# Performance work log

Hardware: AMD Instinct MI355X
Metric: run time of the kernel (lower is better)

## Reference

```python
import jax, jax.numpy as jnp
import numpy as np

NUM_EMBEDDINGS = 1024
EMBEDDING_DIM = 256
COMMITMENT_COST = 0.25


def setup_inputs() -> dict:
    key = jax.random.key(0)
    k1, k2 = jax.random.split(key)
    inputs = jax.random.normal(k1, (32, EMBEDDING_DIM, 32, 32), dtype=jnp.float32)
    # nn.Embedding weight init: uniform(-1/K, 1/K)
    embeddings = (jax.random.uniform(k2, (NUM_EMBEDDINGS, EMBEDDING_DIM), dtype=jnp.float32) * 2.0 - 1.0) / NUM_EMBEDDINGS
    return {"inputs": inputs, "embeddings": embeddings}


def reference(inputs, embeddings):
    B, D, H, W = inputs.shape
    K = embeddings.shape[0]
    # [B,D,H,W] -> [N,D] with N = B*H*W
    flat = jnp.transpose(inputs, (0, 2, 3, 1)).reshape(-1, D)
    distances = (jnp.sum(flat * flat, axis=1, keepdims=True)
                 + jnp.sum(embeddings * embeddings, axis=1)
                 - 2.0 * jnp.matmul(flat, embeddings.T))
    encoding_indices = jnp.argmin(distances, axis=1)  # [N]
    # gather codebook vectors (same math as one-hot @ embeddings)
    quantized = embeddings[encoding_indices]  # [N,D]
    quantized = quantized.reshape(B, H, W, D).transpose(0, 3, 1, 2)  # [B,D,H,W]
    e_latent_loss = jnp.mean((jax.lax.stop_gradient(quantized) - inputs) ** 2)
    q_latent_loss = jnp.mean((quantized - jax.lax.stop_gradient(inputs)) ** 2)
    loss = q_latent_loss + COMMITMENT_COST * e_latent_loss
    # straight-through estimator
    quantized_st = inputs + jax.lax.stop_gradient(quantized - inputs)
    # perplexity from one-hot average (counts / N)
    counts = jnp.zeros((K,), dtype=flat.dtype).at[encoding_indices].add(1.0)
    avg_probs = counts / flat.shape[0]
    perplexity = jnp.exp(-jnp.sum(avg_probs * jnp.log(avg_probs + 1e-10)))
    return quantized_st, loss, perplexity, encoding_indices.reshape(B, H, W)
```

## Files before the change

kernel.cpp:

```cpp
#include <hip/hip_runtime.h>


#define NROWS 32768
#define CAPA 16384
#define CAPB 8192
#define GAP_TAU 1e-4f

typedef __attribute__((ext_vector_type(8))) short short8;
typedef __attribute__((ext_vector_type(8))) unsigned short ushort8;
typedef __attribute__((ext_vector_type(4))) float f32x4;
typedef __attribute__((ext_vector_type(4))) unsigned int uint4v;

struct Top4 { float v0, v1, v2, v3; int i0, i1, i2; };

__device__ __forceinline__ void top4_init(Top4& t) {
    t.v0 = t.v1 = t.v2 = t.v3 = 3.4e38f;
    t.i0 = t.i1 = t.i2 = 0x7fffffff;
}
__device__ __forceinline__ void top4_insert(Top4& t, float cv, int ci) {
    if (cv < t.v3) {
        if (cv < t.v2) {
            t.v3 = t.v2;
            if (cv < t.v1) {
                t.v2 = t.v1; t.i2 = t.i1;
                if (cv < t.v0) { t.v1 = t.v0; t.i1 = t.i0; t.v0 = cv; t.i0 = ci; }
                else           { t.v1 = cv; t.i1 = ci; }
            } else { t.v2 = cv; t.i2 = ci; }
        } else { t.v3 = cv; }
    }
}
__device__ __forceinline__ void top4_merge(Top4& t, const Top4& o) {
    top4_insert(t, o.v0, o.i0);
    top4_insert(t, o.v1, o.i1);
    top4_insert(t, o.v2, o.i2);
    t.v3 = fminf(t.v3, o.v3);
}

__device__ __forceinline__ unsigned short bf16_rne(float v) {
    unsigned int u = __float_as_uint(v);
    return (unsigned short)((u + 0x7fffu + ((u >> 16) & 1u)) >> 16);
}
__device__ __forceinline__ float bf16_to_f(unsigned short h) {
    return __uint_as_float(((unsigned int)h) << 16);
}

template <int STRIDE>
__device__ __forceinline__ float np_sumsq256(const float* __restrict__ p) {
    float half[2];
#pragma unroll
    for (int h = 0; h < 2; ++h) {
        float r[8];
#pragma unroll
        for (int j = 0; j < 8; ++j) {
            const float v = p[(size_t)(h * 128 + j) * STRIDE];
            r[j] = __fmul_rn(v, v);
        }
        for (int i = 8; i < 128; i += 8) {
#pragma unroll
            for (int j = 0; j < 8; ++j) {
                const float v = p[(size_t)(h * 128 + i + j) * STRIDE];
                r[j] = __fadd_rn(r[j], __fmul_rn(v, v));
            }
        }
        half[h] = __fadd_rn(__fadd_rn(__fadd_rn(r[0], r[1]), __fadd_rn(r[2], r[3])),
                            __fadd_rn(__fadd_rn(r[4], r[5]), __fadd_rn(r[6], r[7])));
    }
    return __fadd_rn(half[0], half[1]);
}

__global__ void prep_kernel(const float* __restrict__ emb, const float* __restrict__ x,
                            float* __restrict__ ee, float* __restrict__ xx,
                            unsigned short* __restrict__ EhW, unsigned short* __restrict__ ElW) {
    if (blockIdx.x < 4) {
        const int k = blockIdx.x * 256 + threadIdx.x;
        ee[k] = np_sumsq256<1>(emb + (size_t)k * 256);
        return;
    }
    if (blockIdx.x >= 260) {
        const int n = (blockIdx.x - 260) * 256 + threadIdx.x;
        const int b = n >> 10, p = n & 1023;
        xx[n] = np_sumsq256<1024>(x + (size_t)b * 262144 + p);
        return;
    }
    const int eid = (blockIdx.x - 4) * 256 + threadIdx.x;
    const int base = eid * 4;
    float4 v = *(const float4*)(emb + base);
    const float vv[4] = {v.x, v.y, v.z, v.w};
    unsigned short h[4], l[4];
#pragma unroll
    for (int i = 0; i < 4; ++i) {
        h[i] = bf16_rne(vv[i]);
        l[i] = bf16_rne(vv[i] - bf16_to_f(h[i]));
    }
    *(ushort4*)(EhW + base) = make_ushort4(h[0], h[1], h[2], h[3]);
    *(ushort4*)(ElW + base) = make_ushort4(l[0], l[1], l[2], l[3]);
}

__global__ __launch_bounds__(256, 4)
void mfma_argmin_kernel(const float* __restrict__ x,
                        const unsigned short* __restrict__ EhW, const unsigned short* __restrict__ ElW,
                        const float* __restrict__ ee, const float* __restrict__ xx,
                        float* __restrict__ pv0, float* __restrict__ pv1,
                        float* __restrict__ pv2, float* __restrict__ pv3,
                        int* __restrict__ pi0, int* __restrict__ pi1, int* __restrict__ pi2) {
    __shared__ unsigned short Eh_s[128 * 32];
    __shared__ unsigned short El_s[128 * 32];
    __shared__ unsigned short Xh_s[128 * 32];
    __shared__ unsigned short Xl_s[128 * 32];
    __shared__ float eeLds[128];
    __shared__ float mV0[128], mV1[128], mV2[128], mV3[128];
    __shared__ int   mI0[128], mI1[128], mI2[128];

    const int t = threadIdx.x;
    const int w = t >> 6, lane = t & 63;
    const int lane15 = lane & 15, quad = lane >> 4;
    const int nblk = blockIdx.x & 255, cblk = blockIdx.x >> 8;
    const int n0 = nblk * 128, c0 = cblk * 128;
    const int b = n0 >> 10, p0 = n0 & 1023;
    const float* xb = x + (size_t)b * 262144 + p0;

    if (t < 128) eeLds[t] = ee[c0 + t];

    f32x4 acc[4][4];
#pragma unroll
    for (int i = 0; i < 4; ++i)
#pragma unroll
        for (int j = 0; j < 4; ++j) acc[i][j] = (f32x4){0.f, 0.f, 0.f, 0.f};

    for (int dc = 0; dc < 8; ++dc) {
        const int d0 = dc * 32;
        __syncthreads();
#pragma unroll
        for (int iter = 0; iter < 2; ++iter) {
            const int id = iter * 256 + t;
            const int p = id & 127, dblk = id >> 7;
            const float* src = xb + (size_t)(d0 + dblk * 8) * 1024 + p;
            float v[8];
#pragma unroll
            for (int j = 0; j < 8; ++j) v[j] = src[(size_t)j * 1024];
            uint4v uh, ul;
#pragma unroll
            for (int jj = 0; jj < 4; ++jj) {
                const unsigned int u0 = __float_as_uint(v[2 * jj]);
                const unsigned int u1 = __float_as_uint(v[2 * jj + 1]);
                uh[jj] = __builtin_amdgcn_perm(u1, u0, 0x07060302u);
                const float r0 = v[2 * jj]     - __uint_as_float(u0 & 0xFFFF0000u);
                const float r1 = v[2 * jj + 1] - __uint_as_float(u1 & 0xFFFF0000u);
                ul[jj] = __builtin_amdgcn_perm(__float_as_uint(r1), __float_as_uint(r0), 0x07060302u);
            }
            *(uint4v*)&Xh_s[p * 32 + dblk * 8] = uh;
            *(uint4v*)&Xl_s[p * 32 + dblk * 8] = ul;
        }
#pragma unroll
        for (int iter = 0; iter < 2; ++iter) {
            const int id = iter * 256 + t;
            const int row = id >> 2, col = id & 3;
            const size_t g = (size_t)(c0 + row) * 256 + d0 + col * 8;
            *(ushort8*)&Eh_s[row * 32 + col * 8] = *(const ushort8*)(EhW + g);
            *(ushort8*)&El_s[row * 32 + col * 8] = *(const ushort8*)(ElW + g);
        }
        __syncthreads();
        short8 ah[4], al[4], bhf[4], blf[4];
#pragma unroll
        for (int i = 0; i < 4; ++i) {
            const int cr = (w >> 1) * 64 + i * 16 + lane15;
            ah[i] = *(const short8*)&Eh_s[cr * 32 + quad * 8];
            al[i] = *(const short8*)&El_s[cr * 32 + quad * 8];
        }
#pragma unroll
        for (int j = 0; j < 4; ++j) {
            const int nr = (w & 1) * 64 + j * 16 + lane15;
            bhf[j] = *(const short8*)&Xh_s[nr * 32 + quad * 8];
            blf[j] = *(const short8*)&Xl_s[nr * 32 + quad * 8];
        }
#pragma unroll
        for (int i = 0; i < 4; ++i)
#pragma unroll
            for (int j = 0; j < 4; ++j) {
                acc[i][j] = __builtin_amdgcn_mfma_f32_16x16x32_bf16(al[i], bhf[j], acc[i][j], 0, 0, 0);
                acc[i][j] = __builtin_amdgcn_mfma_f32_16x16x32_bf16(ah[i], blf[j], acc[i][j], 0, 0, 0);
                acc[i][j] = __builtin_amdgcn_mfma_f32_16x16x32_bf16(ah[i], bhf[j], acc[i][j], 0, 0, 0);
            }
    }
    Top4 tj[4];
#pragma unroll
    for (int j = 0; j < 4; ++j) {
        const float xxv = xx[n0 + (w & 1) * 64 + j * 16 + lane15];
        Top4 tt; top4_init(tt);
#pragma unroll
        for (int i = 0; i < 4; ++i)
#pragma unroll
            for (int r = 0; r < 4; ++r) {
                const int cl = (w >> 1) * 64 + i * 16 + quad * 4 + r;
                const float t1 = __fadd_rn(xxv, eeLds[cl]);
                const float s = __fmaf_rn(-2.0f, acc[i][j][r], t1);
                top4_insert(tt, s, c0 + cl);
            }
#pragma unroll
        for (int off = 16; off <= 32; off <<= 1) {
            Top4 o;
            o.v0 = __shfl_xor(tt.v0, off, 64); o.i0 = __shfl_xor(tt.i0, off, 64);
            o.v1 = __shfl_xor(tt.v1, off, 64); o.i1 = __shfl_xor(tt.i1, off, 64);
            o.v2 = __shfl_xor(tt.v2, off, 64); o.i2 = __shfl_xor(tt.i2, off, 64);
            o.v3 = __shfl_xor(tt.v3, off, 64);
            top4_merge(tt, o);
        }
        tj[j] = tt;
    }
    __syncthreads();
    if (w >= 2 && quad == 0) {
#pragma unroll
        for (int j = 0; j < 4; ++j) {
            const int idx = (w & 1) * 64 + j * 16 + lane15;
            mV0[idx] = tj[j].v0; mV1[idx] = tj[j].v1; mV2[idx] = tj[j].v2; mV3[idx] = tj[j].v3;
            mI0[idx] = tj[j].i0; mI1[idx] = tj[j].i1; mI2[idx] = tj[j].i2;
        }
    }
    __syncthreads();
    if (w < 2 && quad == 0) {
#pragma unroll
        for (int j = 0; j < 4; ++j) {
            const int idx = w * 64 + j * 16 + lane15;
            Top4 tt = tj[j];
            Top4 o;
            o.v0 = mV0[idx]; o.v1 = mV1[idx]; o.v2 = mV2[idx]; o.v3 = mV3[idx];
            o.i0 = mI0[idx]; o.i1 = mI1[idx]; o.i2 = mI2[idx];
            top4_merge(tt, o);
            const size_t g = (size_t)cblk * NROWS + n0 + idx;
            pv0[g] = tt.v0; pv1[g] = tt.v1; pv2[g] = tt.v2; pv3[g] = tt.v3;
            pi0[g] = tt.i0; pi1[g] = tt.i1; pi2[g] = tt.i2;
        }
    }
}

__global__ void combine_kernel(const float* __restrict__ pv0, const float* __restrict__ pv1,
                               const float* __restrict__ pv2, const float* __restrict__ pv3,
                               const int* __restrict__ pi0, const int* __restrict__ pi1,
                               const int* __restrict__ pi2,
                               int* __restrict__ fidx, float* __restrict__ outIdx,
                               int* __restrict__ counts,
                               int* __restrict__ listA, int* __restrict__ nA,
                               int* __restrict__ listB, int* __restrict__ nB) {
    const int n = blockIdx.x * blockDim.x + threadIdx.x;
    if (n >= NROWS) return;
    float v0[8], v1[8], v2[8]; int i0[8], i1[8], i2[8];
    float b1 = 3.4e38f, v4m = 3.4e38f;
#pragma unroll
    for (int s = 0; s < 8; ++s) {
        const size_t g = (size_t)s * NROWS + n;
        v0[s] = pv0[g]; v1[s] = pv1[g]; v2[s] = pv2[g];
        i0[s] = pi0[g]; i1[s] = pi1[g]; i2[s] = pi2[g];
        b1 = fminf(b1, v0[s]);
        v4m = fminf(v4m, pv3[g]);
    }
    if (v4m - b1 < GAP_TAU) {
        const int s = atomicAdd(nB, 1);
        if (s < CAPB) { listB[s] = n; return; }
    } else {
        int ks[24]; int cnt = 0;
#pragma unroll
        for (int s = 0; s < 8; ++s) {
            if (v0[s] - b1 < GAP_TAU) ks[cnt++] = i0[s];
            if (v1[s] - b1 < GAP_TAU) ks[cnt++] = i1[s];
            if (v2[s] - b1 < GAP_TAU) ks[cnt++] = i2[s];
        }
        if (cnt > 1) {
            const int slot = atomicAdd(nA, 1);
            if (slot < CAPA) {
                int* e = listA + (size_t)slot * 32;
                e[0] = n; e[1] = cnt;
                for (int c = 0; c < cnt; ++c) e[2 + c] = ks[c];
                return;
            }
            const int s2 = atomicAdd(nB, 1);
            if (s2 < CAPB) { listB[s2] = n; return; }
        }
        const int bi = ks[0];
        fidx[n] = bi;
        outIdx[n] = (float)bi;
        atomicAdd(&counts[bi], 1);
        return;
    }
    int bi = 0x7fffffff;
#pragma unroll
    for (int s = 0; s < 8; ++s) if (v0[s] == b1 && i0[s] < bi) bi = i0[s];
    fidx[n] = bi; outIdx[n] = (float)bi; atomicAdd(&counts[bi], 1);
}

__global__ __launch_bounds__(256)
void exact_kernel(const float* __restrict__ x, const float* __restrict__ emb,
                  const float* __restrict__ ee, const float* __restrict__ xx,
                  const int* __restrict__ listA, const int* __restrict__ nA,
                  int* __restrict__ fidx, float* __restrict__ outIdx,
                  int* __restrict__ counts) {
    int total = *nA; if (total > CAPA) total = CAPA;
    const int sub = threadIdx.x >> 5;
    const int li  = threadIdx.x & 31;
    for (int e = blockIdx.x * 8 + sub; e < total; e += gridDim.x * 8) {
        const int* ent = listA + (size_t)e * 32;
        const int n = ent[0], cnt = ent[1];
        float s = 3.4e38f; int k = 0x7fffffff;
        if (li < cnt) {
            k = ent[2 + li];
            const int b = n >> 10, p = n & 1023;
            const float* xr = x + (size_t)b * 262144 + p;
            const float* er = emb + (size_t)k * 256;
            float dot = 0.f;
#pragma unroll 8
            for (int d = 0; d < 256; ++d)
                dot = __fmaf_rn(er[d], xr[(size_t)d * 1024], dot);
            s = __fmaf_rn(-2.0f, dot, __fadd_rn(xx[n], ee[k]));
        }
#pragma unroll
        for (int off = 1; off < 32; off <<= 1) {
            const float ov = __shfl_xor(s, off, 32);
            const int   ok = __shfl_xor(k, off, 32);
            if (ov < s || (ov == s && ok < k)) { s = ov; k = ok; }
        }
        if (li == 0) { fidx[n] = k; outIdx[n] = (float)k; atomicAdd(&counts[k], 1); }
    }
}

__global__ __launch_bounds__(256)
void rescanB_kernel(const float* __restrict__ x, const float* __restrict__ emb,
                    const float* __restrict__ ee, const float* __restrict__ xx,
                    const int* __restrict__ listB, const int* __restrict__ nB,
                    int* __restrict__ fidx, float* __restrict__ outIdx,
                    int* __restrict__ counts) {
    __shared__ float xrow[256];
    __shared__ float bV[4];
    __shared__ int   bI[4];
    int total = *nB; if (total > CAPB) total = CAPB;
    for (int wq = blockIdx.x; wq < total; wq += gridDim.x) {
        const int n = listB[wq];
        const int b = n >> 10, p = n & 1023;
        const float* xb = x + (size_t)b * 262144 + p;
        xrow[threadIdx.x] = xb[(size_t)threadIdx.x * 1024];
        __syncthreads();
        const float xxn = xx[n];
        float best = 3.4e38f; int bi = 0x7fffffff;
        for (int k = threadIdx.x; k < 1024; k += 256) {
            const float* e = emb + (size_t)k * 256;
            float dot = 0.f;
            for (int d = 0; d < 256; ++d) dot = __fmaf_rn(e[d], xrow[d], dot);
            const float t1 = __fadd_rn(xxn, ee[k]);
            const float s = __fmaf_rn(-2.0f, dot, t1);
            if (s < best) { best = s; bi = k; }
        }
        for (int off = 32; off > 0; off >>= 1) {
            const float ov = __shfl_down(best, off, 64);
            const int   oi = __shfl_down(bi,   off, 64);
            if (ov < best || (ov == best && oi < bi)) { best = ov; bi = oi; }
        }
        const int lane = threadIdx.x & 63, wv = threadIdx.x >> 6;
        if (lane == 0) { bV[wv] = best; bI[wv] = bi; }
        __syncthreads();
        if (threadIdx.x == 0) {
            float bb = bV[0]; int ii = bI[0];
            for (int i = 1; i < 4; ++i)
                if (bV[i] < bb || (bV[i] == bb && bI[i] < ii)) { bb = bV[i]; ii = bI[i]; }
            fidx[n] = ii;
            outIdx[n] = (float)ii;
            atomicAdd(&counts[ii], 1);
        }
        __syncthreads();
    }
}

__global__ __launch_bounds__(256)
void quantize_kernel(const float* __restrict__ x, const float* __restrict__ emb,
                     const int* __restrict__ fidx, float* __restrict__ out,
                     float* __restrict__ sumsq) {
    const int tid = blockIdx.x * 256 + threadIdx.x;
    const int dchunk = tid >> 15;
    const int n = tid & 32767;
    const int b = n >> 10, p = n & 1023;
    const int d0 = dchunk * 64;
    const int k = fidx[n];
    const float4* er = (const float4*)(emb + (size_t)k * 256 + d0);
    const float* xr = x + (size_t)b * 262144 + (size_t)d0 * 1024 + p;
    float* orow = out + (size_t)b * 262144 + (size_t)d0 * 1024 + p;
    float loc = 0.f;
#pragma unroll
    for (int j = 0; j < 16; ++j) {
        const float4 qv = er[j];
        const float q[4] = {qv.x, qv.y, qv.z, qv.w};
#pragma unroll
        for (int i = 0; i < 4; ++i) {
            const size_t off = (size_t)(j * 4 + i) * 1024;
            const float xv = xr[off];
            const float e = q[i] - xv;
            orow[off] = xv + e;
            loc = fmaf(e, e, loc);
        }
    }
    for (int off = 32; off > 0; off >>= 1) loc += __shfl_down(loc, off, 64);
    __shared__ float red[4];
    const int lane = threadIdx.x & 63, wv = threadIdx.x >> 6;
    if (lane == 0) red[wv] = loc;
    __syncthreads();
    if (threadIdx.x == 0) atomicAdd(sumsq, red[0] + red[1] + red[2] + red[3]);
}

__global__ void finalize_kernel(const int* __restrict__ counts, const float* __restrict__ sumsq,
                                float* __restrict__ outScalars) {
    const int k = threadIdx.x;
    const float p = (float)counts[k] * (1.0f / 32768.0f);
    float term = p * logf(p + 1e-10f);
    for (int off = 32; off > 0; off >>= 1) term += __shfl_down(term, off, 64);
    __shared__ float red[16];
    const int lane = k & 63, wv = k >> 6;
    if (lane == 0) red[wv] = term;
    __syncthreads();
    if (k == 0) {
        float s = 0.f;
        for (int i = 0; i < 16; ++i) s += red[i];
        const float m = sumsq[0] * (1.0f / 8388608.0f);
        outScalars[0] = 1.25f * m;
        outScalars[1] = expf(-s);
    }
}

extern "C" void kernel_launch(void* const* d_in, const int* in_sizes, int n_in,
                              void* d_out, int out_size, void* d_ws, size_t ws_size,
                              hipStream_t stream) {
    const float* x   = (const float*)d_in[0];
    const float* emb = (const float*)d_in[1];
    float* out = (float*)d_out;
    float* W   = (float*)d_ws;
    float* sumsq = W;
    int*   nA    = (int*)(W + 1);
    int*   nB    = (int*)(W + 2);
    int*   counts = (int*)(W + 64);
    float* ee    = W + 1088;
    float* xx    = W + 2112;
    float* pv0   = W + 34880;
    float* pv1   = W + 297024;
    float* pv2   = W + 559168;
    float* pv3   = W + 821312;
    int*   pi0   = (int*)(W + 1083456);
    int*   pi1   = (int*)(W + 1345600);
    int*   pi2   = (int*)(W + 1607744);
    int*   listA = (int*)(W + 1869888);
    int*   listB = (int*)(W + 2394176);
    unsigned short* EhW = (unsigned short*)(W + 2402368);
    unsigned short* ElW = (unsigned short*)(W + 2533440);
    int*   fidx  = (int*)(W + 2664512);

    hipMemsetAsync(W, 0, 1088 * sizeof(float), stream);
    prep_kernel<<<388, 256, 0, stream>>>(emb, x, ee, xx, EhW, ElW);
    mfma_argmin_kernel<<<2048, 256, 0, stream>>>(x, EhW, ElW, ee, xx,
                                                 pv0, pv1, pv2, pv3, pi0, pi1, pi2);
    combine_kernel<<<128, 256, 0, stream>>>(pv0, pv1, pv2, pv3, pi0, pi1, pi2,
                                            fidx, out + 8388610, counts, listA, nA, listB, nB);
    exact_kernel<<<512, 256, 0, stream>>>(x, emb, ee, xx, listA, nA, fidx, out + 8388610, counts);
    rescanB_kernel<<<64, 256, 0, stream>>>(x, emb, ee, xx, listB, nB, fidx, out + 8388610, counts);
    quantize_kernel<<<512, 256, 0, stream>>>(x, emb, fidx, out, sumsq);
    finalize_kernel<<<1, 1024, 0, stream>>>(counts, sumsq, out + 8388608);
}
```

Measured before the change: 231.1 us.

## Pre-split inputs to bf16 hi/lo tiles in prep and stream via direct LDS loads

The prep kernel now converts the inputs to bf16 high/low parts once, written in a tile-major [dc][row][32] layout, and also stores the codebook split in the same tiled layout. The MFMA argmin kernel then fills shared memory with global_load_lds 16-byte direct copies instead of reading strided fp32 inputs and converting them per block. This removes the conversion work that was repeated across the eight codebook blocks and the strided loads. In exchange the prep kernel writes an extra 32 MB of workspace, and its xx path now does more register-heavy work.

```diff
diff --git a/kernel.cpp b/kernel.cpp
--- a/kernel.cpp
+++ b/kernel.cpp
@@ -9,7 +9,6 @@
 typedef __attribute__((ext_vector_type(8))) short short8;
 typedef __attribute__((ext_vector_type(8))) unsigned short ushort8;
 typedef __attribute__((ext_vector_type(4))) float f32x4;
-typedef __attribute__((ext_vector_type(4))) unsigned int uint4v;
 
 struct Top4 { float v0, v1, v2, v3; int i0, i1, i2; };
 
@@ -44,6 +43,12 @@
     return __uint_as_float(((unsigned int)h) << 16);
 }
 
+__device__ __forceinline__ void gl16(const void* g, void* l) {
+    __builtin_amdgcn_global_load_lds(
+        (const __attribute__((address_space(1))) unsigned int*)g,
+        (__attribute__((address_space(3))) unsigned int*)l, 16, 0, 0);
+}
+
 template <int STRIDE>
 __device__ __forceinline__ float np_sumsq256(const float* __restrict__ p) {
     float half[2];
@@ -70,7 +75,8 @@
 
 __global__ void prep_kernel(const float* __restrict__ emb, const float* __restrict__ x,
                             float* __restrict__ ee, float* __restrict__ xx,
-                            unsigned short* __restrict__ EhW, unsigned short* __restrict__ ElW) {
+                            unsigned short* __restrict__ EhT, unsigned short* __restrict__ ElT,
+                            unsigned short* __restrict__ XhT, unsigned short* __restrict__ XlT) {
     if (blockIdx.x < 4) {
         const int k = blockIdx.x * 256 + threadIdx.x;
         ee[k] = np_sumsq256<1>(emb + (size_t)k * 256);
@@ -79,12 +85,58 @@
     if (blockIdx.x >= 260) {
         const int n = (blockIdx.x - 260) * 256 + threadIdx.x;
         const int b = n >> 10, p = n & 1023;
-        xx[n] = np_sumsq256<1024>(x + (size_t)b * 262144 + p);
+        const float* xb = x + (size_t)b * 262144 + p;
+        float r[8];
+        float half0 = 0.f, half1 = 0.f;
+        for (int dc = 0; dc < 8; ++dc) {
+            float v[32];
+#pragma unroll
+            for (int j = 0; j < 32; ++j)
+                v[j] = xb[(size_t)(dc * 32 + j) * 1024];
+            if ((dc & 3) == 0) {
+#pragma unroll
+                for (int j = 0; j < 8; ++j) r[j] = __fmul_rn(v[j], v[j]);
+#pragma unroll
+                for (int g = 1; g < 4; ++g)
+#pragma unroll
+                    for (int j = 0; j < 8; ++j)
+                        r[j] = __fadd_rn(r[j], __fmul_rn(v[g * 8 + j], v[g * 8 + j]));
+            } else {
+#pragma unroll
+                for (int g = 0; g < 4; ++g)
+#pragma unroll
+                    for (int j = 0; j < 8; ++j)
+                        r[j] = __fadd_rn(r[j], __fmul_rn(v[g * 8 + j], v[g * 8 + j]));
+            }
+            if ((dc & 3) == 3) {
+                const float s = __fadd_rn(
+                    __fadd_rn(__fadd_rn(r[0], r[1]), __fadd_rn(r[2], r[3])),
+                    __fadd_rn(__fadd_rn(r[4], r[5]), __fadd_rn(r[6], r[7])));
+                if (dc == 3) half0 = s; else half1 = s;
+            }
+            const size_t xrow = ((size_t)dc * NROWS + n) * 32;
+#pragma unroll
+            for (int g = 0; g < 4; ++g) {
+                ushort8 H, L;
+#pragma unroll
+                for (int j = 0; j < 8; ++j) {
+                    const float vv = v[g * 8 + j];
+                    const unsigned int u = __float_as_uint(vv);
+                    H[j] = (unsigned short)(u >> 16);
+                    const float rr = vv - __uint_as_float(u & 0xFFFF0000u);
+                    L[j] = (unsigned short)(__float_as_uint(rr) >> 16);
+                }
+                *(ushort8*)(XhT + xrow + g * 8) = H;
+                *(ushort8*)(XlT + xrow + g * 8) = L;
+            }
+        }
+        xx[n] = __fadd_rn(half0, half1);
         return;
     }
     const int eid = (blockIdx.x - 4) * 256 + threadIdx.x;
-    const int base = eid * 4;
-    float4 v = *(const float4*)(emb + base);
+    const int code = eid >> 6;
+    const int d0 = (eid & 63) * 4;
+    float4 v = *(const float4*)(emb + (size_t)code * 256 + d0);
     const float vv[4] = {v.x, v.y, v.z, v.w};
     unsigned short h[4], l[4];
 #pragma unroll
@@ -92,21 +144,22 @@
         h[i] = bf16_rne(vv[i]);
         l[i] = bf16_rne(vv[i] - bf16_to_f(h[i]));
     }
-    *(ushort4*)(EhW + base) = make_ushort4(h[0], h[1], h[2], h[3]);
-    *(ushort4*)(ElW + base) = make_ushort4(l[0], l[1], l[2], l[3]);
+    const size_t o = ((size_t)(d0 >> 5) * 1024 + code) * 32 + (d0 & 31);
+    *(ushort4*)(EhT + o) = make_ushort4(h[0], h[1], h[2], h[3]);
+    *(ushort4*)(ElT + o) = make_ushort4(l[0], l[1], l[2], l[3]);
 }
 
 __global__ __launch_bounds__(256, 4)
-void mfma_argmin_kernel(const float* __restrict__ x,
-                        const unsigned short* __restrict__ EhW, const unsigned short* __restrict__ ElW,
+void mfma_argmin_kernel(const unsigned short* __restrict__ XhT, const unsigned short* __restrict__ XlT,
+                        const unsigned short* __restrict__ EhT, const unsigned short* __restrict__ ElT,
                         const float* __restrict__ ee, const float* __restrict__ xx,
                         float* __restrict__ pv0, float* __restrict__ pv1,
                         float* __restrict__ pv2, float* __restrict__ pv3,
                         int* __restrict__ pi0, int* __restrict__ pi1, int* __restrict__ pi2) {
-    __shared__ unsigned short Eh_s[128 * 32];
-    __shared__ unsigned short El_s[128 * 32];
-    __shared__ unsigned short Xh_s[128 * 32];
-    __shared__ unsigned short Xl_s[128 * 32];
+    __shared__ __attribute__((aligned(16))) unsigned short Eh_s[128 * 32];
+    __shared__ __attribute__((aligned(16))) unsigned short El_s[128 * 32];
+    __shared__ __attribute__((aligned(16))) unsigned short Xh_s[128 * 32];
+    __shared__ __attribute__((aligned(16))) unsigned short Xl_s[128 * 32];
     __shared__ float eeLds[128];
     __shared__ float mV0[128], mV1[128], mV2[128], mV3[128];
     __shared__ int   mI0[128], mI1[128], mI2[128];
@@ -116,8 +169,6 @@
     const int lane15 = lane & 15, quad = lane >> 4;
     const int nblk = blockIdx.x & 255, cblk = blockIdx.x >> 8;
     const int n0 = nblk * 128, c0 = cblk * 128;
-    const int b = n0 >> 10, p0 = n0 & 1023;
-    const float* xb = x + (size_t)b * 262144 + p0;
 
     if (t < 128) eeLds[t] = ee[c0 + t];
 
@@ -128,36 +179,17 @@
         for (int j = 0; j < 4; ++j) acc[i][j] = (f32x4){0.f, 0.f, 0.f, 0.f};
 
     for (int dc = 0; dc < 8; ++dc) {
-        const int d0 = dc * 32;
-        __syncthreads();
-#pragma unroll
-        for (int iter = 0; iter < 2; ++iter) {
-            const int id = iter * 256 + t;
-            const int p = id & 127, dblk = id >> 7;
-            const float* src = xb + (size_t)(d0 + dblk * 8) * 1024 + p;
-            float v[8];
-#pragma unroll
-            for (int j = 0; j < 8; ++j) v[j] = src[(size_t)j * 1024];
-            uint4v uh, ul;
-#pragma unroll
-            for (int jj = 0; jj < 4; ++jj) {
-                const unsigned int u0 = __float_as_uint(v[2 * jj]);
-                const unsigned int u1 = __float_as_uint(v[2 * jj + 1]);
-                uh[jj] = __builtin_amdgcn_perm(u1, u0, 0x07060302u);
-                const float r0 = v[2 * jj]     - __uint_as_float(u0 & 0xFFFF0000u);
-                const float r1 = v[2 * jj + 1] - __uint_as_float(u1 & 0xFFFF0000u);
-                ul[jj] = __builtin_amdgcn_perm(__float_as_uint(r1), __float_as_uint(r0), 0x07060302u);
-            }
-            *(uint4v*)&Xh_s[p * 32 + dblk * 8] = uh;
-            *(uint4v*)&Xl_s[p * 32 + dblk * 8] = ul;
-        }
-#pragma unroll
-        for (int iter = 0; iter < 2; ++iter) {
-            const int id = iter * 256 + t;
-            const int row = id >> 2, col = id & 3;
-            const size_t g = (size_t)(c0 + row) * 256 + d0 + col * 8;
-            *(ushort8*)&Eh_s[row * 32 + col * 8] = *(const ushort8*)(EhW + g);
-            *(ushort8*)&El_s[row * 32 + col * 8] = *(const ushort8*)(ElW + g);
+        if (dc) __syncthreads();
+        const size_t xoff = ((size_t)dc * NROWS + n0) * 32;
+        const size_t eoff = ((size_t)dc * 1024 + c0) * 32;
+#pragma unroll
+        for (int k = 0; k < 2; ++k) {
+            const int id = k * 256 + t;
+            const int ldso = (k * 256 + w * 64) * 8;
+            gl16(XhT + xoff + (size_t)id * 8, &Xh_s[ldso]);
+            gl16(XlT + xoff + (size_t)id * 8, &Xl_s[ldso]);
+            gl16(EhT + eoff + (size_t)id * 8, &Eh_s[ldso]);
+            gl16(ElT + eoff + (size_t)id * 8, &El_s[ldso]);
         }
         __syncthreads();
         short8 ah[4], al[4], bhf[4], blf[4];
@@ -443,13 +475,15 @@
     int*   pi2   = (int*)(W + 1607744);
     int*   listA = (int*)(W + 1869888);
     int*   listB = (int*)(W + 2394176);
-    unsigned short* EhW = (unsigned short*)(W + 2402368);
-    unsigned short* ElW = (unsigned short*)(W + 2533440);
+    unsigned short* EhT = (unsigned short*)(W + 2402368);
+    unsigned short* ElT = (unsigned short*)(W + 2533440);
     int*   fidx  = (int*)(W + 2664512);
+    unsigned short* XhT = (unsigned short*)(W + 2697280);
+    unsigned short* XlT = (unsigned short*)(W + 6891584);
 
     hipMemsetAsync(W, 0, 1088 * sizeof(float), stream);
-    prep_kernel<<<388, 256, 0, stream>>>(emb, x, ee, xx, EhW, ElW);
-    mfma_argmin_kernel<<<2048, 256, 0, stream>>>(x, EhW, ElW, ee, xx,
+    prep_kernel<<<388, 256, 0, stream>>>(emb, x, ee, xx, EhT, ElT, XhT, XlT);
+    mfma_argmin_kernel<<<2048, 256, 0, stream>>>(XhT, XlT, EhT, ElT, ee, xx,
                                                  pv0, pv1, pv2, pv3, pi0, pi1, pi2);
     combine_kernel<<<128, 256, 0, stream>>>(pv0, pv1, pv2, pv3, pi0, pi1, pi2,
                                             fidx, out + 8388610, counts, listA, nA, listB, nB);
```

Result: faster. 219.2 us (-5.2%).
